# Kernel tuning notes

Measured on AMD Instinct MI355X. Metric: run time of the kernel, lower is better.

Reference implementation:

```python
import jax, jax.numpy as jnp
import numpy as np
from jax import lax

B, N, C = 256, 256, 192
HEADS = 6
HD = C // HEADS
WIN = 16
AGENT = 49
POOL = 7            # int(agent_num ** 0.5)
SCALE = HD ** -0.5


def _pool_matrix(inn, out):
    # PyTorch AdaptiveAvgPool2d bin edges: start=floor(i*inn/out), end=ceil((i+1)*inn/out)
    P = np.zeros((out, inn), np.float32)
    for i in range(out):
        s = (i * inn) // out
        e = -(((-(i + 1)) * inn) // out)
        P[i, s:e] = 1.0 / (e - s)
    return jnp.asarray(P)

_P = _pool_matrix(WIN, POOL)  # (7, 16) adaptive-avg-pool operator


def _resize_bilinear(x, out_h, out_w):
    # matches F.interpolate(mode='bilinear', align_corners=False)
    H, W = x.shape[-2], x.shape[-1]
    def idx(out, inn):
        s = (jnp.arange(out, dtype=jnp.float32) + 0.5) * (inn / out) - 0.5
        s = jnp.maximum(s, 0.0)
        i0 = jnp.minimum(jnp.floor(s).astype(jnp.int32), inn - 1)
        i1 = jnp.minimum(i0 + 1, inn - 1)
        return i0, i1, s - i0.astype(jnp.float32)
    h0, h1, th = idx(out_h, H)
    w0, w1, tw = idx(out_w, W)
    xh = x[..., h0, :] * (1.0 - th)[:, None] + x[..., h1, :] * th[:, None]
    return xh[..., :, w0] * (1.0 - tw) + xh[..., :, w1] * tw


def setup_inputs() -> dict:
    key = jax.random.key(0)
    ks = jax.random.split(key, 18)
    lin = lambda k: jax.random.normal(k, (C, C), jnp.float32) * 0.02
    zc = jnp.zeros((C,), jnp.float32)
    tn = lambda k, shp: jax.random.normal(k, shp, jnp.float32) * 0.02
    return {
        "x_F1": jax.random.normal(ks[0], (B, N, C), jnp.float32),
        "x_C2": jax.random.normal(ks[1], (B, N, C), jnp.float32),
        "x_C1": jax.random.normal(ks[2], (B, N, C), jnp.float32),
        "Wq": lin(ks[3]), "bq": zc,
        "Wk": lin(ks[4]), "bk": zc,
        "Wv": lin(ks[5]), "bv": zc,
        "Wa1": lin(ks[6]), "ba1": zc,
        "Wa2": lin(ks[7]), "ba2": zc,
        "an_bias": tn(ks[8], (HEADS, AGENT, 7, 7)),
        "na_bias": tn(ks[9], (HEADS, AGENT, 7, 7)),
        "ah_bias": tn(ks[10], (1, HEADS, AGENT, WIN, 1)),
        "aw_bias": tn(ks[11], (1, HEADS, AGENT, 1, WIN)),
        "ha_bias": tn(ks[12], (1, HEADS, WIN, 1, AGENT)),
        "wa_bias": tn(ks[13], (1, HEADS, 1, WIN, AGENT)),
        "dwc_w": tn(ks[14], (C, 1, 3, 3)),
        "dwc_b": zc,
        "Wp": lin(ks[15]), "bp": zc,
    }


def reference(x_F1, x_C2, x_C1, Wq, bq, Wk, bk, Wv, bv, Wa1, ba1, Wa2, ba2,
              an_bias, na_bias, ah_bias, aw_bias, ha_bias, wa_bias,
              dwc_w, dwc_b, Wp, bp):
    b, n, c = x_F1.shape
    h = w = WIN
    q = x_F1 @ Wq.T + bq
    k = (x_F1 + x_C2 - x_C1) @ Wk.T + bk
    v = (x_C2 - x_C1) @ Wv.T + bv
    # agent tokens: linear -> adaptive avg pool 16x16 -> 7x7 -> (b, 49, c)
    a1 = (x_C1 @ Wa1.T + ba1).reshape(b, h, w, c)
    a1 = jnp.einsum('ph,bhwc,qw->bpqc', _P, a1, _P).reshape(b, AGENT, c)
    a2 = (x_C2 @ Wa2.T + ba2).reshape(b, h, w, c)
    a2 = jnp.einsum('ph,bhwc,qw->bpqc', _P, a2, _P).reshape(b, AGENT, c)
    qh = q.reshape(b, n, HEADS, HD).transpose(0, 2, 1, 3)
    kh = k.reshape(b, n, HEADS, HD).transpose(0, 2, 1, 3)
    vh = v.reshape(b, n, HEADS, HD).transpose(0, 2, 1, 3)
    a1h = a1.reshape(b, AGENT, HEADS, HD).transpose(0, 2, 1, 3)
    a2h = a2.reshape(b, AGENT, HEADS, HD).transpose(0, 2, 1, 3)
    # stage 1: agent <- k/v attention, bias = interp(an_bias) + (ah+aw)
    pb = (_resize_bilinear(an_bias, h, w).reshape(1, HEADS, AGENT, n)
          + (ah_bias + aw_bias).reshape(1, HEADS, AGENT, n))
    attn2 = jax.nn.softmax(SCALE * jnp.einsum('bhad,bhnd->bhan', a2h, kh) + pb, axis=-1)
    agent_v = jnp.einsum('bhan,bhnd->bhad', attn2, vh)
    # stage 2: query <- agent attention, bias = interp(na_bias)^T + (ha+wa)
    ab = (jnp.swapaxes(_resize_bilinear(na_bias, h, w).reshape(HEADS, AGENT, n), -1, -2)[None]
          + (ha_bias + wa_bias).reshape(1, HEADS, n, AGENT))
    q_attn = jax.nn.softmax(SCALE * jnp.einsum('bhnd,bhad->bhna', qh, a1h) + ab, axis=-1)
    x = jnp.einsum('bhna,bhad->bhnd', q_attn, agent_v).transpose(0, 2, 1, 3).reshape(b, n, c)
    # depthwise 3x3 conv on q as spatial map
    q_img = q.reshape(b, h, w, c).transpose(0, 3, 1, 2)
    dw = lax.conv_general_dilated(q_img, dwc_w, (1, 1), ((1, 1), (1, 1)),
                                  feature_group_count=c,
                                  dimension_numbers=('NCHW', 'OIHW', 'NCHW'))
    dw = dw + dwc_b.reshape(1, c, 1, 1)
    x = x + dw.transpose(0, 2, 3, 1).reshape(b, n, c)
    return x @ Wp.T + bp
```

## Files before the change

kernel.cpp:

```cpp
#include <hip/hip_runtime.h>

typedef __bf16 bf16;
typedef __bf16 bf16x4 __attribute__((ext_vector_type(4)));
typedef __bf16 bf16x8 __attribute__((ext_vector_type(8)));
typedef float  f32x4  __attribute__((ext_vector_type(4)));

#define DEVI __device__ __forceinline__

static constexpr int   BATCH = 256;
static constexpr int   SEQ   = 256;
static constexpr int   CH    = 192;
static constexpr int   NH    = 6;
static constexpr int   AG    = 49;
static constexpr float QK_SCALE = 0.17677669529663687f;

__device__ constexpr int   PPN[16]  = {1,1,2,1,2,1,2,1,1,2,1,2,1,2,1,1};
__device__ constexpr int   PPB0[16] = {0,0,0,1,1,2,2,3,3,3,4,4,5,5,6,6};
__device__ constexpr int   PPB1[16] = {0,0,1,0,2,0,3,0,0,4,0,5,0,6,0,0};
__device__ constexpr float PPW0[16] = {1.f/3.f,1.f/3.f,1.f/3.f,1.f/3.f,1.f/3.f,1.f/3.f,1.f/3.f,0.25f,0.25f,0.25f,
                                       1.f/3.f,1.f/3.f,1.f/3.f,1.f/3.f,1.f/3.f,1.f/3.f};
__device__ constexpr float PPW1[16] = {0.f,0.f,1.f/3.f,0.f,1.f/3.f,0.f,0.25f,0.f,0.f,1.f/3.f,
                                       0.f,1.f/3.f,0.f,1.f/3.f,0.f,0.f};

#if defined(__has_builtin)
#if __has_builtin(__builtin_amdgcn_global_load_lds)
#define HAVE_GLL 1
#endif
#endif

DEVI void gll16(const void* g, void* l, int lane) {
#ifdef HAVE_GLL
  (void)lane;
  __builtin_amdgcn_global_load_lds(
      (const __attribute__((address_space(1))) void*)g,
      (__attribute__((address_space(3))) void*)l, 16, 0, 0);
#else
  *(uint4*)((char*)l + lane * 16) = *(const uint4*)((const char*)g);
#endif
}

DEVI float bilin7(const float* m, int i, int j) {
  float sh = (i + 0.5f) * 0.4375f - 0.5f; sh = sh < 0.f ? 0.f : sh;
  float sw = (j + 0.5f) * 0.4375f - 0.5f; sw = sw < 0.f ? 0.f : sw;
  int i0 = (int)sh; if (i0 > 6) i0 = 6;
  int j0 = (int)sw; if (j0 > 6) j0 = 6;
  int i1 = i0 + 1;  if (i1 > 6) i1 = 6;
  int j1 = j0 + 1;  if (j1 > 6) j1 = 6;
  float th = sh - (float)i0, tw = sw - (float)j0;
  float v00 = m[i0*7 + j0], v01 = m[i0*7 + j1];
  float v10 = m[i1*7 + j0], v11 = m[i1*7 + j1];
  return (v00*(1.f-tw) + v01*tw)*(1.f-th) + (v10*(1.f-tw) + v11*tw)*th;
}

__global__ void k_prep(const float* Wq, const float* Wk, const float* Wv,
                       const float* Wa1, const float* Wa2, const float* Wp,
                       const float* an_bias, const float* na_bias,
                       const float* ah_bias, const float* aw_bias,
                       const float* ha_bias, const float* wa_bias,
                       bf16* wsW, bf16* pb, bf16* ab, bf16* a1, bf16* a2) {
  int gid = blockIdx.x * 256 + threadIdx.x;
  if (gid < 221184) {
    int mi = gid / 36864, r = gid - mi * 36864;
    const float* W = (mi == 0 ? Wq : mi == 1 ? Wk : mi == 2 ? Wv :
                      mi == 3 ? Wa1 : mi == 4 ? Wa2 : Wp);
    wsW[gid] = (bf16)W[r];
  } else if (gid < 296448) {
    int r = gid - 221184;
    int n = r & 255, ha = r >> 8;
    int i = n >> 4, j = n & 15;
    float val = bilin7(an_bias + (size_t)ha * 49, i, j)
              + ah_bias[ha * 16 + i] + aw_bias[ha * 16 + j];
    pb[r] = (bf16)val;
  } else if (gid < 382464) {
    int r = gid - 296448;
    int a = r % 56, hn = r / 56;
    int n = hn & 255, hh = hn >> 8;
    int i = n >> 4, j = n & 15;
    float val = 0.f;
    if (a < AG)
      val = bilin7(na_bias + (size_t)(hh * 49 + a) * 49, i, j)
          + ha_bias[(hh * 16 + i) * 49 + a] + wa_bias[(hh * 16 + j) * 49 + a];
    ab[r] = (bf16)val;
  } else if (gid < 407040) {
    int r = gid - 382464;
    if (r < 12288) a1[(size_t)12544 * CH + r] = (bf16)0.f;
    else           a2[(size_t)12544 * CH + (r - 12288)] = (bf16)0.f;
  }
}

__global__ __launch_bounds__(256, 4) void k_combo(
    const float* xF1, const float* xC2, const float* xC1,
    bf16* f1b, bf16* kin, bf16* vin) {
  const int base = blockIdx.x * 1536 + threadIdx.x;
  #pragma unroll
  for (int g = 0; g < 2; ++g) {
    int rows[3], byts[3];
    float f[3][8], c2[3][8], c1[3][8];
    #pragma unroll
    for (int s = 0; s < 3; ++s) {
      const int slot = base + 256 * (3 * g + s);
      const int row  = slot / 24;
      const int cb   = slot - row * 24;
      rows[s] = row;
      byts[s] = (cb * 16) ^ ((row & 7) << 4);
      const size_t rf = (size_t)row * CH + cb * 8;
      *(float4*)&f[s][0]  = *(const float4*)(xF1 + rf);
      *(float4*)&f[s][4]  = *(const float4*)(xF1 + rf + 4);
      *(float4*)&c2[s][0] = *(const float4*)(xC2 + rf);
      *(float4*)&c2[s][4] = *(const float4*)(xC2 + rf + 4);
      *(float4*)&c1[s][0] = *(const float4*)(xC1 + rf);
      *(float4*)&c1[s][4] = *(const float4*)(xC1 + rf + 4);
    }
    #pragma unroll
    for (int s = 0; s < 3; ++s) {
      bf16x8 tq, tk, tv;
      #pragma unroll
      for (int e = 0; e < 8; ++e) {
        const float d = c2[s][e] - c1[s][e];
        tq[e] = (bf16)f[s][e];
        tk[e] = (bf16)(f[s][e] + d);
        tv[e] = (bf16)d;
      }
      const size_t rowb = (size_t)rows[s] * 384;
      *(bf16x8*)((char*)f1b + rowb + byts[s]) = tq;
      *(bf16x8*)((char*)kin + rowb + byts[s]) = tk;
      *(bf16x8*)((char*)vin + rowb + byts[s]) = tv;
    }
  }
}

__global__ __launch_bounds__(256, 3) void k_gemm3b(
    const bf16* f1b, const bf16* kin, const bf16* vin, const bf16* wsW,
    const float* bq, const float* bk, const float* bv,
    bf16* qO, bf16* kO, bf16* vT) {
  __shared__ char sA[49152] __attribute__((aligned(16)));
  const int tid = threadIdx.x, lane = tid & 63, wid = tid >> 6;
  const int l15 = lane & 15, lg = lane >> 4;
  const int wr = wid >> 1, wc = wid & 1;
  const int job = blockIdx.y;
  const int m0 = blockIdx.x * 128;
  const bf16*  Aj   = (job == 0 ? f1b : job == 1 ? kin : vin);
  const bf16*  Wj   = wsW + job * 36864;
  const float* bias = (job == 0 ? bq : job == 1 ? bk : bv);

  {
    const char* gsrc = (const char*)Aj + (size_t)m0 * 384;
    #pragma unroll
    for (int i = 0; i < 12; ++i) {
      const int off = (wid * 12 + i) * 1024;
      gll16(gsrc + off + lane * 16, sA + off, lane);
    }
  }
  __syncthreads();

  f32x4 acc[4][6];
  #pragma unroll
  for (int a = 0; a < 4; ++a)
    #pragma unroll
    for (int b2 = 0; b2 < 6; ++b2) acc[a][b2] = f32x4{0.f, 0.f, 0.f, 0.f};

  #pragma unroll
  for (int kk = 0; kk < 6; ++kk) {
    bf16x8 af[4];
    #pragma unroll
    for (int rt = 0; rt < 4; ++rt) {
      const int row = 64 * wr + 16 * rt + l15;
      af[rt] = *(const bf16x8*)(sA + row * 384 + ((kk * 64 + lg * 16) ^ ((row & 7) << 4)));
    }
    #pragma unroll
    for (int ct = 0; ct < 6; ++ct) {
      const int ncol = 96 * wc + 16 * ct + l15;
      bf16x8 bfr = *(const bf16x8*)&Wj[(size_t)ncol * CH + kk * 32 + 8 * lg];
      #pragma unroll
      for (int rt = 0; rt < 4; ++rt)
        acc[rt][ct] = __builtin_amdgcn_mfma_f32_16x16x32_bf16(af[rt], bfr, acc[rt][ct], 0, 0, 0);
    }
  }
  __syncthreads();

  if (job < 2) {
    bf16* outp = (job == 0 ? qO : kO);
    #pragma unroll
    for (int ct = 0; ct < 6; ++ct) {
      const int col = 96 * wc + 16 * ct + l15;
      const float bb = bias[col];
      #pragma unroll
      for (int rt = 0; rt < 4; ++rt)
        #pragma unroll
        for (int r = 0; r < 4; ++r) {
          const int row = 64 * wr + 16 * rt + 4 * lg + r;
          *(bf16*)(sA + row * 384 + ((2 * col) ^ ((row & 7) << 4))) = (bf16)(acc[rt][ct][r] + bb);
        }
    }
    __syncthreads();
    #pragma unroll
    for (int g = 0; g < 12; ++g) {
      const int ch  = tid + 256 * g;
      const int row = ch / 24;
      const int y   = (ch - row * 24) * 16;
      bf16x8 vv = *(const bf16x8*)(sA + row * 384 + (y ^ ((row & 7) << 4)));
      *(bf16x8*)((char*)outp + (size_t)(m0 + row) * 384 + y) = vv;
    }
  } else {
    #pragma unroll
    for (int ct = 0; ct < 6; ++ct) {
      const int col = 96 * wc + 16 * ct + l15;
      const float bb = bias[col];
      #pragma unroll
      for (int rt = 0; rt < 4; ++rt)
        #pragma unroll
        for (int r = 0; r < 4; ++r) {
          const int row = 64 * wr + 16 * rt + 4 * lg + r;
          const int byt = col * 256 + (((2 * row) & ~15) ^ ((col & 7) << 4)) + ((2 * row) & 15);
          *(bf16*)(sA + byt) = (bf16)(acc[rt][ct][r] + bb);
        }
    }
    __syncthreads();
    const int batch = m0 >> 8, nb = m0 & 255;
    #pragma unroll
    for (int g = 0; g < 12; ++g) {
      const int ch = tid + 256 * g;
      const int c = ch >> 4, o = ch & 15;
      bf16x8 vv = *(const bf16x8*)(sA + c * 256 + ((o * 16) ^ ((c & 7) << 4)));
      *(bf16x8*)(vT + (((size_t)batch * NH + (c >> 5)) * 32 + (c & 31)) * 256 + nb + 8 * o) = vv;
    }
  }
}

#define POOLROW(I, P0, W0, P1, W1) do {                                        \
    float jqx[7] = {0,0,0,0,0,0,0}, jqy[7] = {0,0,0,0,0,0,0};                  \
    _Pragma("unroll")                                                          \
    for (int j = 0; j < 16; ++j) {                                             \
      float2 x = *(const float2*)(src + (size_t)((I) * 16 + j) * CH);          \
      jqx[PPB0[j]] += PPW0[j] * x.x;  jqy[PPB0[j]] += PPW0[j] * x.y;           \
      if (PPN[j] == 2) { jqx[PPB1[j]] += PPW1[j] * x.x;                        \
                         jqy[PPB1[j]] += PPW1[j] * x.y; }                      \
    }                                                                          \
    _Pragma("unroll")                                                          \
    for (int q = 0; q < 7; ++q) { ax[P0][q] += (W0) * jqx[q];                  \
                                  ay[P0][q] += (W0) * jqy[q]; }                \
    if ((P1) >= 0) {                                                           \
      _Pragma("unroll")                                                        \
      for (int q = 0; q < 7; ++q) { ax[(P1) & 3][q] += (W1) * jqx[q];          \
                                    ay[(P1) & 3][q] += (W1) * jqy[q]; }        \
    }                                                                          \
  } while (0)

__global__ __launch_bounds__(192) void k_pool(
    const float* xC1, const float* xC2, bf16* pooled1, bf16* pooled2) {
  __shared__ float lred[7][192];
  const int b = blockIdx.x, which = blockIdx.y, t = threadIdx.x;
  const int cp = t % 96, ih = t / 96;
  const float* src = (which ? xC2 : xC1) + (size_t)b * SEQ * CH + 2 * cp;
  bf16* dst = (which ? pooled2 : pooled1) + (size_t)b * AG * CH + 2 * cp;

  float ax[4][7], ay[4][7];
  #pragma unroll
  for (int p = 0; p < 4; ++p)
    #pragma unroll
    for (int q = 0; q < 7; ++q) { ax[p][q] = 0.f; ay[p][q] = 0.f; }

  const float TH = 1.f / 3.f, QU = 0.25f;
  if (ih == 0) {
    POOLROW(0, 0, TH, -1, 0.f);  POOLROW(1, 0, TH, -1, 0.f);
    POOLROW(2, 0, TH,  1, TH);   POOLROW(3, 1, TH, -1, 0.f);
    POOLROW(4, 1, TH,  2, TH);   POOLROW(5, 2, TH, -1, 0.f);
    POOLROW(6, 2, TH,  3, QU);   POOLROW(7, 3, QU, -1, 0.f);
  } else {
    POOLROW(8,  0, QU, -1, 0.f); POOLROW(9,  0, QU,  1, TH);
    POOLROW(10, 1, TH, -1, 0.f); POOLROW(11, 1, TH,  2, TH);
    POOLROW(12, 2, TH, -1, 0.f); POOLROW(13, 2, TH,  3, TH);
    POOLROW(14, 3, TH, -1, 0.f); POOLROW(15, 3, TH, -1, 0.f);
  }
  if (ih == 1) {
    #pragma unroll
    for (int q = 0; q < 7; ++q) {
      lred[q][2 * cp] = ax[0][q]; lred[q][2 * cp + 1] = ay[0][q];
    }
  }
  __syncthreads();
  if (ih == 0) {
    #pragma unroll
    for (int q = 0; q < 7; ++q) {
      ax[3][q] += lred[q][2 * cp]; ay[3][q] += lred[q][2 * cp + 1];
    }
    #pragma unroll
    for (int p = 0; p < 4; ++p)
      #pragma unroll
      for (int q = 0; q < 7; ++q) {
        union { bf16 e[2]; unsigned u; } u;
        u.e[0] = (bf16)ax[p][q]; u.e[1] = (bf16)ay[p][q];
        *(unsigned*)&dst[(size_t)(p * 7 + q) * CH] = u.u;
      }
  } else {
    #pragma unroll
    for (int lp = 1; lp < 4; ++lp)
      #pragma unroll
      for (int q = 0; q < 7; ++q) {
        union { bf16 e[2]; unsigned u; } u;
        u.e[0] = (bf16)ax[lp][q]; u.e[1] = (bf16)ay[lp][q];
        *(unsigned*)&dst[(size_t)((3 + lp) * 7 + q) * CH] = u.u;
      }
  }
}

DEVI void gemm_body(const bf16* Asrc, const bf16* W, const float* bias,
                    bf16* outp, int m0, bf16 (*sA)[72]) {
  const int tid = threadIdx.x, lane = tid & 63, wid = tid >> 6;
  const int l15 = lane & 15, lg = lane >> 4;
  const int wr = wid >> 1, wc = wid & 1;
  const int srow = tid >> 1, shalf = tid & 1;

  f32x4 acc[4][6];
  #pragma unroll
  for (int a = 0; a < 4; ++a)
    #pragma unroll
    for (int b2 = 0; b2 < 6; ++b2) acc[a][b2] = f32x4{0.f, 0.f, 0.f, 0.f};

  for (int ks = 0; ks < 3; ++ks) {
    const int k0 = ks * 64;
    const uint4* src = (const uint4*)(Asrc + (size_t)(m0 + srow) * CH + k0 + shalf * 32);
    #pragma unroll
    for (int i2 = 0; i2 < 4; ++i2)
      *(uint4*)&sA[srow][shalf * 32 + 8 * i2] = src[i2];
    __syncthreads();
    #pragma unroll
    for (int kk = 0; kk < 64; kk += 32) {
      bf16x8 af[4];
      #pragma unroll
      for (int rt = 0; rt < 4; ++rt)
        af[rt] = *(const bf16x8*)&sA[64 * wr + 16 * rt + l15][kk + 8 * lg];
      #pragma unroll
      for (int ct = 0; ct < 6; ++ct) {
        const int ncol = 96 * wc + 16 * ct + l15;
        bf16x8 bfr = *(const bf16x8*)&W[(size_t)ncol * CH + k0 + kk + 8 * lg];
        #pragma unroll
        for (int rt = 0; rt < 4; ++rt)
          acc[rt][ct] = __builtin_amdgcn_mfma_f32_16x16x32_bf16(af[rt], bfr, acc[rt][ct], 0, 0, 0);
      }
    }
    __syncthreads();
  }
  #pragma unroll
  for (int ct = 0; ct < 6; ++ct) {
    const int col = 96 * wc + 16 * ct + l15;
    const float bb = bias[col];
    #pragma unroll
    for (int rt = 0; rt < 4; ++rt) {
      const size_t rbase = (size_t)(m0 + 64 * wr + 16 * rt + 4 * lg);
      #pragma unroll
      for (int r = 0; r < 4; ++r)
        outp[(rbase + r) * CH + col] = (bf16)(acc[rt][ct][r] + bb);
    }
  }
}

__global__ __launch_bounds__(256, 2) void k_gemm2(
    const bf16* pooled1, const bf16* pooled2, const bf16* wsW,
    const float* ba1, const float* ba2, bf16* a1, bf16* a2) {
  __shared__ bf16 sA[128][72] __attribute__((aligned(16)));
  const int m0 = blockIdx.x * 128;
  if (blockIdx.y == 0) gemm_body(pooled1, wsW + 3 * 36864, ba1, a1, m0, sA);
  else                 gemm_body(pooled2, wsW + 4 * 36864, ba2, a2, m0, sA);
}

__global__ __launch_bounds__(256, 3) void k_gemm_out(
    const bf16* xsum, const bf16* Wp, const float* bp, float* out) {
  __shared__ char sA[49152] __attribute__((aligned(16)));
  const int tid = threadIdx.x, lane = tid & 63, wid = tid >> 6;
  const int l15 = lane & 15, lg = lane >> 4;
  const int wr = wid >> 1, wc = wid & 1;
  const int m0 = blockIdx.x * 128;

  {
    const char* gsrc = (const char*)xsum + (size_t)m0 * 384;
    #pragma unroll
    for (int i = 0; i < 12; ++i) {
      const int off = (wid * 12 + i) * 1024;
      gll16(gsrc + off + lane * 16, sA + off, lane);
    }
  }
  __syncthreads();

  f32x4 acc[4][6];
  #pragma unroll
  for (int a = 0; a < 4; ++a)
    #pragma unroll
    for (int b2 = 0; b2 < 6; ++b2) acc[a][b2] = f32x4{0.f, 0.f, 0.f, 0.f};

  #pragma unroll
  for (int kk = 0; kk < 6; ++kk) {
    bf16x8 af[4];
    #pragma unroll
    for (int rt = 0; rt < 4; ++rt) {
      const int row = 64 * wr + 16 * rt + l15;
      af[rt] = *(const bf16x8*)(sA + row * 384 + ((kk * 64 + lg * 16) ^ ((row & 7) << 4)));
    }
    #pragma unroll
    for (int ct = 0; ct < 6; ++ct) {
      const int ncol = 96 * wc + 16 * ct + l15;
      bf16x8 bfr = *(const bf16x8*)&Wp[(size_t)ncol * CH + kk * 32 + 8 * lg];
      #pragma unroll
      for (int rt = 0; rt < 4; ++rt)
        acc[rt][ct] = __builtin_amdgcn_mfma_f32_16x16x32_bf16(af[rt], bfr, acc[rt][ct], 0, 0, 0);
    }
  }
  #pragma unroll
  for (int ct = 0; ct < 6; ++ct) {
    const int col = 96 * wc + 16 * ct + l15;
    const float bb = bp[col];
    #pragma unroll
    for (int rt = 0; rt < 4; ++rt)
      #pragma unroll
      for (int r = 0; r < 4; ++r)
        out[(size_t)(m0 + 64 * wr + 16 * rt + 4 * lg + r) * CH + col] = acc[rt][ct][r] + bb;
  }
}

__global__ __launch_bounds__(256, 4) void k_attn(
    const bf16* q, const bf16* k, const bf16* vT,
    const bf16* a1, const bf16* a2, const bf16* pb, const bf16* ab,
    const float* dwc_w, const float* dwc_b, bf16* xsum) {
  const int h = blockIdx.x, b = blockIdx.y;
  __shared__ char SM[40960] __attribute__((aligned(16)));
  bf16  (*log1)[264] = reinterpret_cast<bf16 (*)[264]>(SM);
  bf16  (*log2)[56]  = reinterpret_cast<bf16 (*)[56]>(SM);
  bf16  (*sAVT)[72]  = reinterpret_cast<bf16 (*)[72]>(SM + 33792);
  float* srow1       = reinterpret_cast<float*>(SM + 38400);
  float* srow2       = reinterpret_cast<float*>(SM + 38656);
  float (*sW)[32]    = reinterpret_cast<float (*)[32]>(SM + 39680);
  float* dwb         = reinterpret_cast<float*>(SM + 40832);

  const int tid = threadIdx.x, lane = tid & 63, wv = tid >> 6;
  const int l15 = lane & 15, lg = lane >> 4;

  const bf16* qb  = q  + (size_t)b * SEQ * CH + h * 32;
  const bf16* kb  = k  + (size_t)b * SEQ * CH + h * 32;
  const bf16* vTb = vT + ((size_t)(b * NH + h) * 32) * 256;
  const bf16* a1b = a1 + (size_t)b * AG  * CH + h * 32;
  const bf16* a2b = a2 + (size_t)b * AG  * CH + h * 32;

  for (int idx = tid; idx < 288; idx += 256) {
    const int cl = idx / 9, tap = idx - cl * 9;
    sW[tap][cl] = dwc_w[(32 * h + cl) * 9 + tap];
  }
  if (tid < 32) dwb[tid] = dwc_b[32 * h + tid];

  {
    bf16x8 afr[4];
    #pragma unroll
    for (int rt = 0; rt < 4; ++rt)
      afr[rt] = *(const bf16x8*)(a2b + (size_t)(16 * rt + l15) * CH + 8 * lg);
    #pragma unroll
    for (int ct = 0; ct < 4; ++ct) {
      const int n = 64 * wv + 16 * ct + l15;
      bf16x8 bfr = *(const bf16x8*)(kb + (size_t)n * CH + 8 * lg);
      #pragma unroll
      for (int rt = 0; rt < 4; ++rt) {
        f32x4 acc = {0.f, 0.f, 0.f, 0.f};
        acc = __builtin_amdgcn_mfma_f32_16x16x32_bf16(afr[rt], bfr, acc, 0, 0, 0);
        #pragma unroll
        for (int r = 0; r < 4; ++r)
          log1[16 * rt + 4 * lg + r][n] = (bf16)acc[r];
      }
    }
  }
  __syncthreads();

  if (tid < 196) {
    const int a = tid >> 2, qu = tid & 3;
    const bf16* pbrow = pb + ((size_t)h * AG + a) * SEQ + qu * 64;
    float m = -1e30f;
    #pragma unroll
    for (int i2 = 0; i2 < 8; ++i2) {
      bf16x8 raw = *(const bf16x8*)&log1[a][qu * 64 + 8 * i2];
      bf16x8 pbb = *(const bf16x8*)&pbrow[8 * i2];
      #pragma unroll
      for (int j = 0; j < 8; ++j)
        m = fmaxf(m, QK_SCALE * (float)raw[j] + (float)pbb[j]);
    }
    m = fmaxf(m, __shfl_xor(m, 1));
    m = fmaxf(m, __shfl_xor(m, 2));
    float s = 0.f;
    #pragma unroll
    for (int i2 = 0; i2 < 8; ++i2) {
      bf16x8 raw = *(const bf16x8*)&log1[a][qu * 64 + 8 * i2];
      bf16x8 pbb = *(const bf16x8*)&pbrow[8 * i2];
      bf16x8 eb;
      #pragma unroll
      for (int j = 0; j < 8; ++j) {
        float e = __expf(QK_SCALE * (float)raw[j] + (float)pbb[j] - m);
        s += e;
        eb[j] = (bf16)e;
      }
      *(bf16x8*)&log1[a][qu * 64 + 8 * i2] = eb;
    }
    s += __shfl_xor(s, 1);
    s += __shfl_xor(s, 2);
    if (qu == 0) srow1[a] = 1.f / s;
  }

  {
    f32x4 acc0 = {0.f, 0.f, 0.f, 0.f}, acc1 = {0.f, 0.f, 0.f, 0.f};
    #pragma unroll
    for (int ksn = 0; ksn < 8; ++ksn) {
      bf16x8 af = *(const bf16x8*)&log1[16 * wv + l15][32 * ksn + 8 * lg];
      bf16x8 b0 = *(const bf16x8*)(vTb + (size_t)l15 * 256 + 32 * ksn + 8 * lg);
      bf16x8 b1 = *(const bf16x8*)(vTb + (size_t)(16 + l15) * 256 + 32 * ksn + 8 * lg);
      acc0 = __builtin_amdgcn_mfma_f32_16x16x32_bf16(af, b0, acc0, 0, 0, 0);
      acc1 = __builtin_amdgcn_mfma_f32_16x16x32_bf16(af, b1, acc1, 0, 0, 0);
    }
    #pragma unroll
    for (int r = 0; r < 4; ++r) {
      const int a = 16 * wv + 4 * lg + r;
      const float inv = (a < AG) ? srow1[a] : 0.f;
      sAVT[l15][a]      = (bf16)(acc0[r] * inv);
      sAVT[16 + l15][a] = (bf16)(acc1[r] * inv);
    }
  }
  __syncthreads();

  {
    bf16x8 bfr[4];
    #pragma unroll
    for (int ct = 0; ct < 4; ++ct)
      bfr[ct] = *(const bf16x8*)(a1b + (size_t)(16 * ct + l15) * CH + 8 * lg);
    #pragma unroll
    for (int rt = 0; rt < 4; ++rt) {
      bf16x8 af = *(const bf16x8*)(qb + (size_t)(64 * wv + 16 * rt + l15) * CH + 8 * lg);
      #pragma unroll
      for (int ct = 0; ct < 4; ++ct) {
        f32x4 acc = {0.f, 0.f, 0.f, 0.f};
        acc = __builtin_amdgcn_mfma_f32_16x16x32_bf16(af, bfr[ct], acc, 0, 0, 0);
        if (ct < 3 || l15 == 0) {
          #pragma unroll
          for (int r = 0; r < 4; ++r)
            log2[64 * wv + 16 * rt + 4 * lg + r][16 * ct + l15] = (bf16)acc[r];
        }
      }
    }
  }

  {
    const bf16* abrow = ab + ((size_t)h * SEQ + tid) * 56;
    float m = -1e30f;
    #pragma unroll
    for (int i2 = 0; i2 < 6; ++i2) {
      bf16x8 raw = *(const bf16x8*)&log2[tid][8 * i2];
      bf16x8 abb = *(const bf16x8*)&abrow[8 * i2];
      #pragma unroll
      for (int j = 0; j < 8; ++j)
        m = fmaxf(m, QK_SCALE * (float)raw[j] + (float)abb[j]);
    }
    m = fmaxf(m, QK_SCALE * (float)log2[tid][48] + (float)abrow[48]);
    float s = 0.f;
    #pragma unroll
    for (int i2 = 0; i2 < 6; ++i2) {
      bf16x8 raw = *(const bf16x8*)&log2[tid][8 * i2];
      bf16x8 abb = *(const bf16x8*)&abrow[8 * i2];
      bf16x8 eb;
      #pragma unroll
      for (int j = 0; j < 8; ++j) {
        float e = __expf(QK_SCALE * (float)raw[j] + (float)abb[j] - m);
        s += e;
        eb[j] = (bf16)e;
      }
      *(bf16x8*)&log2[tid][8 * i2] = eb;
    }
    {
      float e48 = __expf(QK_SCALE * (float)log2[tid][48] + (float)abrow[48] - m);
      s += e48;
      bf16x8 eb;
      eb[0] = (bf16)e48;
      #pragma unroll
      for (int j = 1; j < 8; ++j) eb[j] = (bf16)0.f;
      *(bf16x8*)&log2[tid][48] = eb;
    }
    srow2[tid] = 1.f / s;
  }

  {
    bf16x8 bfr[2][2];
    #pragma unroll
    for (int ksn = 0; ksn < 2; ++ksn) {
      bfr[ksn][0] = *(const bf16x8*)&sAVT[l15][32 * ksn + 8 * lg];
      bfr[ksn][1] = *(const bf16x8*)&sAVT[16 + l15][32 * ksn + 8 * lg];
    }
    #pragma unroll
    for (int rt = 0; rt < 4; ++rt) {
      f32x4 acc0 = {0.f, 0.f, 0.f, 0.f}, acc1 = {0.f, 0.f, 0.f, 0.f};
      #pragma unroll
      for (int ksn = 0; ksn < 2; ++ksn) {
        bf16x8 af = *(const bf16x8*)&log2[64 * wv + 16 * rt + l15][32 * ksn + 8 * lg];
        acc0 = __builtin_amdgcn_mfma_f32_16x16x32_bf16(af, bfr[ksn][0], acc0, 0, 0, 0);
        acc1 = __builtin_amdgcn_mfma_f32_16x16x32_bf16(af, bfr[ksn][1], acc1, 0, 0, 0);
      }
      #pragma unroll
      for (int r = 0; r < 4; ++r) {
        const int nq = 64 * wv + 16 * rt + 4 * lg + r;
        const float inv = srow2[nq];
        log2[nq][l15]      = (bf16)(acc0[r] * inv);
        log2[nq][16 + l15] = (bf16)(acc1[r] * inv);
      }
    }
  }

  {
    const int n = tid, ii = n >> 4, jj = n & 15;
    float acc[32];
    #pragma unroll
    for (int u = 0; u < 4; ++u) {
      bf16x4 xa0 = *(const bf16x4*)&log2[n][8 * u];
      bf16x4 xa1 = *(const bf16x4*)&log2[n][8 * u + 4];
      #pragma unroll
      for (int e = 0; e < 4; ++e) {
        acc[8 * u + e]     = dwb[8 * u + e]     + (float)xa0[e];
        acc[8 * u + 4 + e] = dwb[8 * u + 4 + e] + (float)xa1[e];
      }
    }
    #pragma unroll
    for (int di = 0; di < 3; ++di) {
      const int i2 = ii + di - 1;
      if ((unsigned)i2 >= 16u) continue;
      #pragma unroll
      for (int dj = 0; dj < 3; ++dj) {
        const int j2 = jj + dj - 1;
        if ((unsigned)j2 >= 16u) continue;
        const int tap = di * 3 + dj;
        const bf16* qr = q + ((size_t)b * SEQ + i2 * 16 + j2) * CH + h * 32;
        #pragma unroll
        for (int u = 0; u < 4; ++u) {
          bf16x8 qv = *(const bf16x8*)(qr + 8 * u);
          const float4* wv4 = (const float4*)&sW[tap][8 * u];
          float4 wa = wv4[0], wb2 = wv4[1];
          acc[8*u+0] += (float)qv[0] * wa.x;  acc[8*u+1] += (float)qv[1] * wa.y;
          acc[8*u+2] += (float)qv[2] * wa.z;  acc[8*u+3] += (float)qv[3] * wa.w;
          acc[8*u+4] += (float)qv[4] * wb2.x; acc[8*u+5] += (float)qv[5] * wb2.y;
          acc[8*u+6] += (float)qv[6] * wb2.z; acc[8*u+7] += (float)qv[7] * wb2.w;
        }
      }
    }
    char* xo = (char*)xsum + (size_t)(b * SEQ + n) * 384;
    const int sw = (n & 7) << 4;
    #pragma unroll
    for (int u = 0; u < 4; ++u) {
      bf16x8 ob;
      #pragma unroll
      for (int e = 0; e < 8; ++e) ob[e] = (bf16)acc[8 * u + e];
      *(bf16x8*)(xo + ((64 * h + 16 * u) ^ sw)) = ob;
    }
  }
}

extern "C" void kernel_launch(void* const* d_in, const int* in_sizes, int n_in,
                              void* d_out, int out_size, void* d_ws, size_t ws_size,
                              hipStream_t stream) {
  (void)in_sizes; (void)n_in; (void)out_size; (void)ws_size;
  const float* xF1 = (const float*)d_in[0];
  const float* xC2 = (const float*)d_in[1];
  const float* xC1 = (const float*)d_in[2];
  const float* Wq  = (const float*)d_in[3];
  const float* bq  = (const float*)d_in[4];
  const float* Wk  = (const float*)d_in[5];
  const float* bk  = (const float*)d_in[6];
  const float* Wv  = (const float*)d_in[7];
  const float* bv  = (const float*)d_in[8];
  const float* Wa1 = (const float*)d_in[9];
  const float* ba1 = (const float*)d_in[10];
  const float* Wa2 = (const float*)d_in[11];
  const float* ba2 = (const float*)d_in[12];
  const float* an_bias = (const float*)d_in[13];
  const float* na_bias = (const float*)d_in[14];
  const float* ah_bias = (const float*)d_in[15];
  const float* aw_bias = (const float*)d_in[16];
  const float* ha_bias = (const float*)d_in[17];
  const float* wa_bias = (const float*)d_in[18];
  const float* dwc_w = (const float*)d_in[19];
  const float* dwc_b = (const float*)d_in[20];
  const float* Wp  = (const float*)d_in[21];
  const float* bp  = (const float*)d_in[22];

  char* ws = (char*)d_ws;
  size_t off = 0;
  auto nxt = [&](size_t bytes) -> char* {
    char* p = ws + off;
    off = (off + bytes + 255) & ~(size_t)255;
    return p;
  };
  const size_t XSZ = (size_t)BATCH * SEQ * CH;
  const size_t ASZ = ((size_t)BATCH * AG + 64) * CH;

  bf16*  wsW     = (bf16*)nxt(6 * 36864 * sizeof(bf16));
  bf16*  pb      = (bf16*)nxt(6 * 49 * 256 * sizeof(bf16));
  bf16*  ab      = (bf16*)nxt(6 * 256 * 56 * sizeof(bf16));
  bf16*  pooled1 = (bf16*)nxt(ASZ * sizeof(bf16));
  bf16*  pooled2 = (bf16*)nxt(ASZ * sizeof(bf16));
  bf16*  f1b     = (bf16*)nxt(XSZ * sizeof(bf16));
  bf16*  kin     = (bf16*)nxt(XSZ * sizeof(bf16));
  bf16*  vin     = (bf16*)nxt(XSZ * sizeof(bf16));
  bf16*  qB      = (bf16*)nxt(XSZ * sizeof(bf16));
  bf16*  kB      = (bf16*)nxt(XSZ * sizeof(bf16));
  bf16*  vTB     = (bf16*)nxt(XSZ * sizeof(bf16));
  bf16*  a1B     = (bf16*)nxt(ASZ * sizeof(bf16));
  bf16*  a2B     = (bf16*)nxt(ASZ * sizeof(bf16));
  bf16*  xsum    = kin;

  k_prep<<<1590, 256, 0, stream>>>(Wq, Wk, Wv, Wa1, Wa2, Wp,
                                   an_bias, na_bias, ah_bias, aw_bias,
                                   ha_bias, wa_bias, wsW, pb, ab, a1B, a2B);
  k_combo<<<1024, 256, 0, stream>>>(xF1, xC2, xC1, f1b, kin, vin);
  k_gemm3b<<<dim3(512, 3), 256, 0, stream>>>(f1b, kin, vin, wsW, bq, bk, bv, qB, kB, vTB);
  k_pool<<<dim3(BATCH, 2), 192, 0, stream>>>(xC1, xC2, pooled1, pooled2);
  k_gemm2<<<dim3(98, 2), 256, 0, stream>>>(pooled1, pooled2, wsW, ba1, ba2, a1B, a2B);
  k_attn<<<dim3(NH, BATCH), 256, 0, stream>>>(qB, kB, vTB, a1B, a2B, pb, ab,
                                              dwc_w, dwc_b, xsum);
  k_gemm_out<<<512, 256, 0, stream>>>(xsum, wsW + 5 * 36864, bp, (float*)d_out);
}
```

Before: 232.7 us.

## Split depthwise conv out of attention kernel into separate LDS-tiled kernel

```diff
diff --git a/kernel.cpp b/kernel.cpp
--- a/kernel.cpp
+++ b/kernel.cpp
@@ -420,16 +420,14 @@
 __global__ __launch_bounds__(256, 4) void k_attn(
     const bf16* q, const bf16* k, const bf16* vT,
     const bf16* a1, const bf16* a2, const bf16* pb, const bf16* ab,
-    const float* dwc_w, const float* dwc_b, bf16* xsum) {
+    bf16* xattnH) {
   const int h = blockIdx.x, b = blockIdx.y;
-  __shared__ char SM[40960] __attribute__((aligned(16)));
+  __shared__ char SM[39680] __attribute__((aligned(16)));
   bf16  (*log1)[264] = reinterpret_cast<bf16 (*)[264]>(SM);
   bf16  (*log2)[56]  = reinterpret_cast<bf16 (*)[56]>(SM);
   bf16  (*sAVT)[72]  = reinterpret_cast<bf16 (*)[72]>(SM + 33792);
   float* srow1       = reinterpret_cast<float*>(SM + 38400);
   float* srow2       = reinterpret_cast<float*>(SM + 38656);
-  float (*sW)[32]    = reinterpret_cast<float (*)[32]>(SM + 39680);
-  float* dwb         = reinterpret_cast<float*>(SM + 40832);
 
   const int tid = threadIdx.x, lane = tid & 63, wv = tid >> 6;
   const int l15 = lane & 15, lg = lane >> 4;
@@ -439,12 +437,6 @@
   const bf16* vTb = vT + ((size_t)(b * NH + h) * 32) * 256;
   const bf16* a1b = a1 + (size_t)b * AG  * CH + h * 32;
   const bf16* a2b = a2 + (size_t)b * AG  * CH + h * 32;
-
-  for (int idx = tid; idx < 288; idx += 256) {
-    const int cl = idx / 9, tap = idx - cl * 9;
-    sW[tap][cl] = dwc_w[(32 * h + cl) * 9 + tap];
-  }
-  if (tid < 32) dwb[tid] = dwc_b[32 * h + tid];
 
   {
     bf16x8 afr[4];
@@ -606,17 +598,65 @@
   }
 
   {
-    const int n = tid, ii = n >> 4, jj = n & 15;
-    float acc[32];
+    bf16* dst = xattnH + ((size_t)(b * NH + h)) * SEQ * 32;
     #pragma unroll
     for (int u = 0; u < 4; ++u) {
-      bf16x4 xa0 = *(const bf16x4*)&log2[n][8 * u];
-      bf16x4 xa1 = *(const bf16x4*)&log2[n][8 * u + 4];
-      #pragma unroll
-      for (int e = 0; e < 4; ++e) {
-        acc[8 * u + e]     = dwb[8 * u + e]     + (float)xa0[e];
-        acc[8 * u + 4 + e] = dwb[8 * u + 4 + e] + (float)xa1[e];
-      }
+      const int ch  = 256 * wv + 64 * u + lane;
+      const int row = ch >> 2, qr = ch & 3;
+      bf16x8 vv = *(const bf16x8*)&log2[row][8 * qr];
+      *(bf16x8*)(dst + (size_t)ch * 8) = vv;
+    }
+  }
+}
+
+DEVI void fma8(float* acc, bf16x8 qv, float4 wa, float4 wb) {
+  acc[0] += (float)qv[0] * wa.x; acc[1] += (float)qv[1] * wa.y;
+  acc[2] += (float)qv[2] * wa.z; acc[3] += (float)qv[3] * wa.w;
+  acc[4] += (float)qv[4] * wb.x; acc[5] += (float)qv[5] * wb.y;
+  acc[6] += (float)qv[6] * wb.z; acc[7] += (float)qv[7] * wb.w;
+}
+
+__global__ __launch_bounds__(256) void k_dwconv(
+    const bf16* q, const bf16* xattnH, const float* dwc_w, const float* dwc_b,
+    bf16* xsum) {
+  __shared__ bf16 sQ[144][200] __attribute__((aligned(16)));
+  __shared__ float sW[9][192] __attribute__((aligned(16)));
+  const int half = blockIdx.x, b = blockIdx.y;
+  const int t = threadIdx.x;
+  const int base_n = half ? 112 : 0;
+
+  if (t < 144) {
+    const bf16* qs = q + ((size_t)b * SEQ + base_n + t) * CH;
+    #pragma unroll
+    for (int i2 = 0; i2 < 24; ++i2)
+      *(uint4*)&sQ[t][8 * i2] = ((const uint4*)qs)[i2];
+  }
+  for (int idx = t; idx < 9 * 192; idx += 256) {
+    int cc = idx / 9, tap = idx - cc * 9;
+    sW[tap][cc] = dwc_w[idx];
+  }
+  __syncthreads();
+
+  const int nloc = t & 127, chalf = t >> 7;
+  const int n = half * 128 + nloc;
+  const int ii = n >> 4, jj = n & 15;
+  const bf16* xaB = xattnH + (size_t)b * NH * SEQ * 32;
+  char* xo = (char*)xsum + (size_t)(b * SEQ + n) * 384;
+  const int sw = (n & 7) << 4;
+  const int c_base = chalf * 96;
+
+  for (int c0 = c_base; c0 < c_base + 96; c0 += 8) {
+    float accv[8];
+    {
+      const float4* bsrc = (const float4*)(dwc_b + c0);
+      float4 b0 = bsrc[0], b1 = bsrc[1];
+      accv[0] = b0.x; accv[1] = b0.y; accv[2] = b0.z; accv[3] = b0.w;
+      accv[4] = b1.x; accv[5] = b1.y; accv[6] = b1.z; accv[7] = b1.w;
+    }
+    {
+      bf16x8 xv = *(const bf16x8*)(xaB + ((size_t)(c0 >> 5) * SEQ + n) * 32 + (c0 & 31));
+      #pragma unroll
+      for (int j = 0; j < 8; ++j) accv[j] += (float)xv[j];
     }
     #pragma unroll
     for (int di = 0; di < 3; ++di) {
@@ -626,29 +666,16 @@
       for (int dj = 0; dj < 3; ++dj) {
         const int j2 = jj + dj - 1;
         if ((unsigned)j2 >= 16u) continue;
-        const int tap = di * 3 + dj;
-        const bf16* qr = q + ((size_t)b * SEQ + i2 * 16 + j2) * CH + h * 32;
-        #pragma unroll
-        for (int u = 0; u < 4; ++u) {
-          bf16x8 qv = *(const bf16x8*)(qr + 8 * u);
-          const float4* wv4 = (const float4*)&sW[tap][8 * u];
-          float4 wa = wv4[0], wb2 = wv4[1];
-          acc[8*u+0] += (float)qv[0] * wa.x;  acc[8*u+1] += (float)qv[1] * wa.y;
-          acc[8*u+2] += (float)qv[2] * wa.z;  acc[8*u+3] += (float)qv[3] * wa.w;
-          acc[8*u+4] += (float)qv[4] * wb2.x; acc[8*u+5] += (float)qv[5] * wb2.y;
-          acc[8*u+6] += (float)qv[6] * wb2.z; acc[8*u+7] += (float)qv[7] * wb2.w;
-        }
-      }
-    }
-    char* xo = (char*)xsum + (size_t)(b * SEQ + n) * 384;
-    const int sw = (n & 7) << 4;
-    #pragma unroll
-    for (int u = 0; u < 4; ++u) {
-      bf16x8 ob;
-      #pragma unroll
-      for (int e = 0; e < 8; ++e) ob[e] = (bf16)acc[8 * u + e];
-      *(bf16x8*)(xo + ((64 * h + 16 * u) ^ sw)) = ob;
-    }
+        const int nn = i2 * 16 + j2 - base_n;
+        bf16x8 qv = *(const bf16x8*)&sQ[nn][c0];
+        const float4* wv4 = (const float4*)&sW[di * 3 + dj][c0];
+        fma8(accv, qv, wv4[0], wv4[1]);
+      }
+    }
+    bf16x8 ob;
+    #pragma unroll
+    for (int j = 0; j < 8; ++j) ob[j] = (bf16)accv[j];
+    *(bf16x8*)(xo + ((2 * c0) ^ sw)) = ob;
   }
 }
 
@@ -703,6 +730,7 @@
   bf16*  vTB     = (bf16*)nxt(XSZ * sizeof(bf16));
   bf16*  a1B     = (bf16*)nxt(ASZ * sizeof(bf16));
   bf16*  a2B     = (bf16*)nxt(ASZ * sizeof(bf16));
+  bf16*  xattnH  = f1b;
   bf16*  xsum    = kin;
 
   k_prep<<<1590, 256, 0, stream>>>(Wq, Wk, Wv, Wa1, Wa2, Wp,
@@ -712,7 +740,7 @@
   k_gemm3b<<<dim3(512, 3), 256, 0, stream>>>(f1b, kin, vin, wsW, bq, bk, bv, qB, kB, vTB);
   k_pool<<<dim3(BATCH, 2), 192, 0, stream>>>(xC1, xC2, pooled1, pooled2);
   k_gemm2<<<dim3(98, 2), 256, 0, stream>>>(pooled1, pooled2, wsW, ba1, ba2, a1B, a2B);
-  k_attn<<<dim3(NH, BATCH), 256, 0, stream>>>(qB, kB, vTB, a1B, a2B, pb, ab,
-                                              dwc_w, dwc_b, xsum);
+  k_attn<<<dim3(NH, BATCH), 256, 0, stream>>>(qB, kB, vTB, a1B, a2B, pb, ab, xattnH);
+  k_dwconv<<<dim3(2, BATCH), 256, 0, stream>>>(qB, xattnH, dwc_w, dwc_b, xsum);
   k_gemm_out<<<512, 256, 0, stream>>>(xsum, wsW + 5 * 36864, bp, (float*)d_out);
 }
```

Result: slower. 238.8 us (+2.6%).
